# Performance work log

Measured on AMD Instinct MI355X. Metric: run time of the kernel, lower is better.

## Reference

```python
import jax, jax.numpy as jnp
import numpy as np

EMBED_DIM = 400          # d; entity embedding is 2d (alpha|beta)
N_ENTITY = 100000
N_RELATION = 500
HIDDEN = 1600
BATCH = 8192


def _reg(x):
    # Regularizer(base_add=1, min_val=0.05, max_val=1e9)
    return jnp.clip(x + 1.0, 0.05, 1e9)


def setup_inputs() -> dict:
    key = jax.random.key(0)
    ks = jax.random.split(key, 16)
    d = EMBED_DIM
    rng = (9.0 + 2.0) / d  # (gamma + epsilon) / embed_dim with gamma=9

    def xavier(k, shape):
        fan_out, fan_in = shape
        lim = np.sqrt(6.0 / (fan_in + fan_out))
        return jax.random.uniform(k, shape, jnp.float32, -lim, lim)

    inp = {
        "anchor1_idx": jax.random.randint(ks[0], (BATCH,), 0, N_ENTITY),
        "rel1_idx": jax.random.randint(ks[1], (BATCH,), 0, N_RELATION),
        "anchor2_idx": jax.random.randint(ks[2], (BATCH,), 0, N_ENTITY),
        "rel2_idx": jax.random.randint(ks[3], (BATCH,), 0, N_RELATION),
        # embedding tables
        "entity_embedding": jax.random.uniform(ks[4], (N_ENTITY, 2 * d), jnp.float32, -rng, rng),
        "relation_embedding": jax.random.uniform(ks[5], (N_RELATION, d), jnp.float32, -rng, rng),
        # BetaProjection: layer1 [hidden, 2d+d], layer2 [hidden, hidden], layer0 [2d, hidden]
        "pW1": xavier(ks[6], (HIDDEN, 3 * d)),
        "pb1": jnp.zeros((HIDDEN,), jnp.float32),
        "pW2": xavier(ks[7], (HIDDEN, HIDDEN)),
        "pb2": jnp.zeros((HIDDEN,), jnp.float32),
        "pW0": xavier(ks[8], (2 * d, HIDDEN)),
        "pb0": jnp.zeros((2 * d,), jnp.float32),
        # BetaIntersection: layer1 [2d, 2d], layer2 [d, 2d]
        "iW1": xavier(ks[9], (2 * d, 2 * d)),
        "ib1": jnp.zeros((2 * d,), jnp.float32),
        "iW2": xavier(ks[10], (d, 2 * d)),
        "ib2": jnp.zeros((d,), jnp.float32),
    }
    return inp


def _projection(e_emb, r_emb, pW1, pb1, pW2, pb2, pW0, pb0):
    # cat -> Linear+ReLU (layer1) -> Linear+ReLU (layer2) -> layer0 -> regularizer
    x = jnp.concatenate([e_emb, r_emb], axis=-1)           # [B, 3d]
    x = jax.nn.relu(x @ pW1.T + pb1)                       # [B, H]
    x = jax.nn.relu(x @ pW2.T + pb2)                       # [B, H]
    x = x @ pW0.T + pb0                                    # [B, 2d]
    return _reg(x)


def _intersection(alphas, betas, iW1, ib1, iW2, ib2):
    # alphas/betas: [K, B, d]; softmax attention over K
    all_emb = jnp.concatenate([alphas, betas], axis=-1)    # [K, B, 2d]
    h = jax.nn.relu(all_emb @ iW1.T + ib1)                 # [K, B, 2d]
    att = jax.nn.softmax(h @ iW2.T + ib2, axis=0)          # [K, B, d]
    return jnp.sum(att * alphas, axis=0), jnp.sum(att * betas, axis=0)


def reference(anchor1_idx, rel1_idx, anchor2_idx, rel2_idx,
              entity_embedding, relation_embedding,
              pW1, pb1, pW2, pb2, pW0, pb0,
              iW1, ib1, iW2, ib2):
    h = _reg(entity_embedding)                             # entity_regularizer
    r = relation_embedding

    emb1 = _projection(h[anchor1_idx], r[rel1_idx], pW1, pb1, pW2, pb2, pW0, pb0)
    a1, b1 = jnp.split(emb1, 2, axis=-1)
    emb2 = _projection(h[anchor2_idx], r[rel2_idx], pW1, pb1, pW2, pb2, pW0, pb0)
    a2, b2 = jnp.split(emb2, 2, axis=-1)

    alpha, beta = _intersection(jnp.stack([a1, a2]), jnp.stack([b1, b2]),
                                iW1, ib1, iW2, ib2)
    return alpha, beta
```

## Files before the change

### kernel.cpp

```cpp
#include <hip/hip_runtime.h>
#include <hip/hip_bf16.h>
#include <stdint.h>

typedef __bf16 bf16_t;
typedef __bf16 bf16x8 __attribute__((ext_vector_type(8)));
typedef float f32x4 __attribute__((ext_vector_type(4)));

constexpr int BATCH = 8192;
constexpr int M = 2 * BATCH;

constexpr int K1 = 1216;
constexpr int N1c = 1792, N1s = 1664;
constexpr int LDA2 = 1664, KL2 = 1600;
constexpr int N2c = 1792, N2s = 1664;
constexpr int LDA3 = 1664, KL3 = 1600;
constexpr int N3c = 1024, N3s = 1024;
constexpr int LDA4 = 1024, KL4 = 832;
constexpr int N4c = 1024, N4s = 1024;
constexpr int LDA5 = 1024, KL5 = 832, N5 = 512;

__device__ __forceinline__ void gload_lds16(const void* g, void* l) {
  __builtin_amdgcn_global_load_lds(
      (const __attribute__((address_space(1))) void*)g,
      (__attribute__((address_space(3))) void*)l,
      16, 0, 0);
}

#define CFENCE() asm volatile("" ::: "memory")
#define BAR()  { CFENCE(); __builtin_amdgcn_s_barrier(); CFENCE(); }

__global__ void gather_kernel(const int* __restrict__ a1, const int* __restrict__ r1,
                              const int* __restrict__ a2, const int* __restrict__ r2,
                              const float* __restrict__ ent, const float* __restrict__ rel,
                              bf16_t* __restrict__ X) {
  const int row = blockIdx.x;
  const int b   = row & (BATCH - 1);
  const int br  = row >> 13;
  const int eidx = br ? a2[b] : a1[b];
  const int ridx = br ? r2[b] : r1[b];
  const float* __restrict__ esrc = ent + (size_t)eidx * 800;
  const float* __restrict__ rsrc = rel + (size_t)ridx * 400;
  bf16_t* __restrict__ dst = X + (size_t)row * K1;

  for (int g = threadIdx.x; g < K1 / 4; g += 256) {
    const int c = g * 4;
    float4 v = make_float4(0.f, 0.f, 0.f, 0.f);
    if (c < 800) {
      v = *(const float4*)(esrc + c);
      v.x = fminf(fmaxf(v.x + 1.f, 0.05f), 1e9f);
      v.y = fminf(fmaxf(v.y + 1.f, 0.05f), 1e9f);
      v.z = fminf(fmaxf(v.z + 1.f, 0.05f), 1e9f);
      v.w = fminf(fmaxf(v.w + 1.f, 0.05f), 1e9f);
    } else if (c < 1200) {
      v = *(const float4*)(rsrc + (c - 800));
    }
    union { bf16_t h[4]; uint2 u; } pk;
    pk.h[0] = (bf16_t)v.x; pk.h[1] = (bf16_t)v.y;
    pk.h[2] = (bf16_t)v.z; pk.h[3] = (bf16_t)v.w;
    *(uint2*)(dst + c) = pk.u;
  }
}

__device__ __forceinline__ void doconv(int idx, const float* __restrict__ src,
                                       bf16_t* __restrict__ dst, int Nr, int Kc, int Kp) {
  const int kp4 = Kp >> 2;
  const int r = idx / kp4;
  const int c = (idx - r * kp4) << 2;
  union { bf16_t h[4]; uint2 u; } pk;
#pragma unroll
  for (int j = 0; j < 4; ++j) {
    const int cc = c + j;
    const float v = (r < Nr && cc < Kc) ? src[(size_t)r * Kc + cc] : 0.f;
    pk.h[j] = (bf16_t)v;
  }
  *(uint2*)(dst + (size_t)r * Kp + c) = pk.u;
}

constexpr int CJ0 = N1c * K1 / 4;
constexpr int CJ1 = CJ0 + N2c * LDA2 / 4;
constexpr int CJ2 = CJ1 + N3c * LDA3 / 4;
constexpr int CJ3 = CJ2 + N4c * LDA4 / 4;
constexpr int CJ4 = CJ3 + N5 * LDA5 / 4;

__global__ void convw5_kernel(const float* __restrict__ pW1, const float* __restrict__ pW2,
                              const float* __restrict__ pW0, const float* __restrict__ iW1,
                              const float* __restrict__ iW2,
                              bf16_t* __restrict__ W1b, bf16_t* __restrict__ W2b,
                              bf16_t* __restrict__ W0b, bf16_t* __restrict__ iW1b,
                              bf16_t* __restrict__ iW2b) {
  int idx = blockIdx.x * 256 + threadIdx.x;
  if (idx < CJ0)      doconv(idx,        pW1, W1b, 1600, 1200, K1);
  else if (idx < CJ1) doconv(idx - CJ0,  pW2, W2b, 1600, 1600, LDA2);
  else if (idx < CJ2) doconv(idx - CJ1,  pW0, W0b,  800, 1600, LDA3);
  else if (idx < CJ3) doconv(idx - CJ2,  iW1, iW1b, 800,  800, LDA4);
  else                doconv(idx - CJ3,  iW2, iW2b, 400,  800, LDA5);
}

enum { ACT_RELU = 0, ACT_REG = 1, ACT_NONE = 2 };

template <int ACT, int OUTMODE>
__global__ __launch_bounds__(512)
void gemm256(const bf16_t* __restrict__ A, const bf16_t* __restrict__ Bw,
             const float* __restrict__ bias, int Nbias,
             bf16_t* __restrict__ Cb, float* __restrict__ Cf,
             int lda, int Nstore, int NT, int gridN) {
  __shared__ __align__(16) bf16_t lds[8][8192];

  const int nwg = gridDim.x;
  const int id = blockIdx.x;
  const int swz = (id & 7) * (nwg >> 3) + (id >> 3);
  const int bn = swz % gridN, bm = swz / gridN;

  const int t = threadIdx.x;
  const int lane = t & 63;
  const int wv = t >> 6;
  const int wm = wv >> 2, wn = wv & 3;
  const int l15 = lane & 15;
  const int kbs = (((lane >> 4) ^ ((l15 >> 1) & 3)) << 4);

  const int srow = t >> 2;
  const int skc  = (t & 3) ^ ((t >> 3) & 3);
  const bf16_t* aR0 = A  + (size_t)(bm * 256 + srow) * lda + skc * 8;
  const bf16_t* aR1 = aR0 + (size_t)128 * lda;
  const bf16_t* bR0 = Bw + (size_t)(bn * 256 + srow) * lda + skc * 8;
  const bf16_t* bR1 = bR0 + (size_t)128 * lda;
  const int ldsb0 = (wv * 64) * 16;
  const int ldsb1 = (512 + wv * 64) * 16;

  auto STAGE = [&](const bf16_t* r0p, const bf16_t* r1p, int kOff, bf16_t* slot) {
    gload_lds16(r0p + kOff, (char*)slot + ldsb0);
    gload_lds16(r1p + kOff, (char*)slot + ldsb1);
  };

  f32x4 acc[8][4];
#pragma unroll
  for (int i = 0; i < 8; ++i)
#pragma unroll
    for (int j = 0; j < 4; ++j) acc[i][j] = f32x4{0.f, 0.f, 0.f, 0.f};

  STAGE(aR0, aR1, 0, lds[0]);
  STAGE(bR0, bR1, 0, lds[2]);
  STAGE(aR0, aR1, 32, lds[1]);
  STAGE(bR0, bR1, 32, lds[3]);
  if (NT > 1) {
    STAGE(aR0, aR1, 64, lds[4]);
    STAGE(bR0, bR1, 64, lds[6]);
    asm volatile("s_waitcnt vmcnt(8)" ::: "memory");
  } else {
    asm volatile("s_waitcnt vmcnt(4)" ::: "memory");
  }
  __builtin_amdgcn_s_barrier();
  CFENCE();

  bf16x8 bfr[4];
  int db = 0;
  for (int kt = 0; kt < NT; ++kt, db ^= 1) {
    const bool p1 = (kt + 1) < NT;
    const bool p2 = (kt + 2) < NT;
    bf16_t* const cur = (bf16_t*)lds[db * 4];
    bf16_t* const nxt = (bf16_t*)lds[(db ^ 1) * 4];

    {
      const char* sA = (const char*)(cur);
      const char* sB = (const char*)(cur + 2 * 8192);
      bf16x8 af[4];
#pragma unroll
      for (int i = 0; i < 4; ++i)
        af[i] = *(const bf16x8*)(sA + ((wm * 128 + i * 16 + l15) << 6) + kbs);
#pragma unroll
      for (int i = 0; i < 4; ++i)
        bfr[i] = *(const bf16x8*)(sB + ((wn * 64 + i * 16 + l15) << 6) + kbs);
      if (p1) STAGE(aR0, aR1, (kt + 1) * 64 + 32, nxt + 1 * 8192);
      BAR();
      __builtin_amdgcn_s_setprio(1);
#pragma unroll
      for (int i = 0; i < 4; ++i)
#pragma unroll
        for (int j = 0; j < 4; ++j)
          acc[i][j] = __builtin_amdgcn_mfma_f32_16x16x32_bf16(af[i], bfr[j], acc[i][j], 0, 0, 0);
      __builtin_amdgcn_s_setprio(0);
      BAR();
    }
    {
      const char* sA = (const char*)(cur);
      bf16x8 af[4];
#pragma unroll
      for (int i = 0; i < 4; ++i)
        af[i] = *(const bf16x8*)(sA + ((wm * 128 + (4 + i) * 16 + l15) << 6) + kbs);
      if (p1) STAGE(bR0, bR1, (kt + 1) * 64 + 32, nxt + 3 * 8192);
      BAR();
      __builtin_amdgcn_s_setprio(1);
#pragma unroll
      for (int i = 0; i < 4; ++i)
#pragma unroll
        for (int j = 0; j < 4; ++j)
          acc[4 + i][j] = __builtin_amdgcn_mfma_f32_16x16x32_bf16(af[i], bfr[j], acc[4 + i][j], 0, 0, 0);
      __builtin_amdgcn_s_setprio(0);
      if (p1) asm volatile("s_waitcnt vmcnt(8)" ::: "memory");
      else    asm volatile("s_waitcnt vmcnt(0)" ::: "memory");
      BAR();
    }
    {
      const char* sA = (const char*)(cur + 1 * 8192);
      const char* sB = (const char*)(cur + 3 * 8192);
      bf16x8 af[4];
#pragma unroll
      for (int i = 0; i < 4; ++i)
        af[i] = *(const bf16x8*)(sA + ((wm * 128 + i * 16 + l15) << 6) + kbs);
#pragma unroll
      for (int i = 0; i < 4; ++i)
        bfr[i] = *(const bf16x8*)(sB + ((wn * 64 + i * 16 + l15) << 6) + kbs);
      if (p2) STAGE(aR0, aR1, (kt + 2) * 64, cur + 0 * 8192);
      BAR();
      __builtin_amdgcn_s_setprio(1);
#pragma unroll
      for (int i = 0; i < 4; ++i)
#pragma unroll
        for (int j = 0; j < 4; ++j)
          acc[i][j] = __builtin_amdgcn_mfma_f32_16x16x32_bf16(af[i], bfr[j], acc[i][j], 0, 0, 0);
      __builtin_amdgcn_s_setprio(0);
      BAR();
    }
    {
      const char* sA = (const char*)(cur + 1 * 8192);
      bf16x8 af[4];
#pragma unroll
      for (int i = 0; i < 4; ++i)
        af[i] = *(const bf16x8*)(sA + ((wm * 128 + (4 + i) * 16 + l15) << 6) + kbs);
      if (p2) STAGE(bR0, bR1, (kt + 2) * 64, cur + 2 * 8192);
      BAR();
      __builtin_amdgcn_s_setprio(1);
#pragma unroll
      for (int i = 0; i < 4; ++i)
#pragma unroll
        for (int j = 0; j < 4; ++j)
          acc[4 + i][j] = __builtin_amdgcn_mfma_f32_16x16x32_bf16(af[i], bfr[j], acc[4 + i][j], 0, 0, 0);
      __builtin_amdgcn_s_setprio(0);
      if (p1) {
        if (p2) asm volatile("s_waitcnt vmcnt(8)" ::: "memory");
        else    asm volatile("s_waitcnt vmcnt(4)" ::: "memory");
      }
      BAR();
    }
  }

  const int r0 = bm * 256 + wm * 128 + ((lane >> 4) * 4);
  const int c0 = bn * 256 + wn * 64 + l15;
#pragma unroll
  for (int ni = 0; ni < 4; ++ni) {
    const int col = c0 + ni * 16;
    const float bv = (col < Nbias) ? bias[col] : 0.f;
    const bool cok = (col < Nstore);
#pragma unroll
    for (int mi = 0; mi < 8; ++mi) {
#pragma unroll
      for (int j = 0; j < 4; ++j) {
        float v = acc[mi][ni][j] + bv;
        if (ACT == ACT_RELU) v = fmaxf(v, 0.f);
        else if (ACT == ACT_REG) v = fminf(fmaxf(v + 1.f, 0.05f), 1e9f);
        if (cok) {
          const size_t off = (size_t)(r0 + mi * 16 + j) * Nstore + col;
          if (OUTMODE == 0 || OUTMODE == 2) Cb[off] = (bf16_t)v;
          if (OUTMODE == 1 || OUTMODE == 2) Cf[off] = v;
        }
      }
    }
  }
}

template <int ACT, int OUTMODE>
__global__ __launch_bounds__(256)
void gemm_kernel(const bf16_t* __restrict__ A, const bf16_t* __restrict__ Bw,
                 const float* __restrict__ bias, int Nbias,
                 bf16_t* __restrict__ Cb, float* __restrict__ Cf,
                 int lda, int Kloop, int Nd) {
  __shared__ __align__(16) bf16_t As[128 * 64];
  __shared__ __align__(16) bf16_t Bs[128 * 64];

  const int bn = blockIdx.x, bm = blockIdx.y;
  const int t = threadIdx.x;
  const int lane = t & 63;
  const int wv = t >> 6;
  const int wm = wv >> 1, wn = wv & 1;

  f32x4 acc[4][4];
#pragma unroll
  for (int i = 0; i < 4; ++i)
#pragma unroll
    for (int j = 0; j < 4; ++j) acc[i][j] = f32x4{0.f, 0.f, 0.f, 0.f};

  const size_t aBase = (size_t)(bm * 128) * lda;
  const size_t bBase = (size_t)(bn * 128) * lda;

  for (int kt = 0; kt < Kloop; kt += 64) {
    __syncthreads();
#pragma unroll
    for (int q = 0; q < 4; ++q) {
      const int lin = q * 256 + t;
      const int row = lin >> 3;
      const int kc = ((lin & 7) ^ ((lin >> 3) & 7)) * 8;
      const int lofs = (q * 256 + wv * 64) * 16;
      gload_lds16(A + aBase + (size_t)row * lda + kt + kc, (char*)As + lofs);
      gload_lds16(Bw + bBase + (size_t)row * lda + kt + kc, (char*)Bs + lofs);
    }
    __syncthreads();

#pragma unroll
    for (int s = 0; s < 2; ++s) {
      const int crd = s * 4 + (lane >> 4);
      const int k0 = (crd ^ (lane & 7)) * 8;
      bf16x8 af[4], bf[4];
#pragma unroll
      for (int i = 0; i < 4; ++i) {
        const int ra = wm * 64 + i * 16 + (lane & 15);
        af[i] = *(const bf16x8*)(As + ra * 64 + k0);
        const int rb = wn * 64 + i * 16 + (lane & 15);
        bf[i] = *(const bf16x8*)(Bs + rb * 64 + k0);
      }
#pragma unroll
      for (int mi = 0; mi < 4; ++mi)
#pragma unroll
        for (int ni = 0; ni < 4; ++ni)
          acc[mi][ni] = __builtin_amdgcn_mfma_f32_16x16x32_bf16(af[mi], bf[ni], acc[mi][ni], 0, 0, 0);
    }
  }

  const int r0 = bm * 128 + wm * 64 + ((lane >> 4) * 4);
  const int c0 = bn * 128 + wn * 64 + (lane & 15);
#pragma unroll
  for (int ni = 0; ni < 4; ++ni) {
    const int col = c0 + ni * 16;
    const float bv = (col < Nbias) ? bias[col] : 0.f;
#pragma unroll
    for (int mi = 0; mi < 4; ++mi) {
#pragma unroll
      for (int j = 0; j < 4; ++j) {
        float v = acc[mi][ni][j] + bv;
        if (ACT == ACT_RELU) v = fmaxf(v, 0.f);
        else if (ACT == ACT_REG) v = fminf(fmaxf(v + 1.f, 0.05f), 1e9f);
        const size_t off = (size_t)(r0 + mi * 16 + j) * Nd + col;
        if (OUTMODE == 0 || OUTMODE == 2) Cb[off] = (bf16_t)v;
        if (OUTMODE == 1 || OUTMODE == 2) Cf[off] = v;
      }
    }
  }
}

__global__ void combine_kernel(const float* __restrict__ L, const float* __restrict__ E,
                               float* __restrict__ out) {
  const int i = blockIdx.x * 256 + threadIdx.x;
  const int b = i / 400;
  const int d = i - b * 400;
  const float l1 = L[(size_t)b * N5 + d];
  const float l2 = L[(size_t)(BATCH + b) * N5 + d];
  const float att1 = 1.f / (1.f + expf(l2 - l1));
  const float att2 = 1.f - att1;
  const float* E1 = E + (size_t)b * N3s;
  const float* E2 = E + (size_t)(BATCH + b) * N3s;
  out[i] = att1 * E1[d] + att2 * E2[d];
  out[(size_t)BATCH * 400 + i] = att1 * E1[400 + d] + att2 * E2[400 + d];
}

extern "C" void kernel_launch(void* const* d_in, const int* in_sizes, int n_in,
                              void* d_out, int out_size, void* d_ws, size_t ws_size,
                              hipStream_t stream) {
  const int* a1 = (const int*)d_in[0];
  const int* r1 = (const int*)d_in[1];
  const int* a2 = (const int*)d_in[2];
  const int* r2 = (const int*)d_in[3];
  const float* ent = (const float*)d_in[4];
  const float* rel = (const float*)d_in[5];
  const float* pW1 = (const float*)d_in[6];
  const float* pb1 = (const float*)d_in[7];
  const float* pW2 = (const float*)d_in[8];
  const float* pb2 = (const float*)d_in[9];
  const float* pW0 = (const float*)d_in[10];
  const float* pb0 = (const float*)d_in[11];
  const float* iW1 = (const float*)d_in[12];
  const float* ib1 = (const float*)d_in[13];
  const float* iW2 = (const float*)d_in[14];
  const float* ib2 = (const float*)d_in[15];

  char* ws = (char*)d_ws;
  size_t o = 0;
  auto take = [&](size_t bytes) { char* p = ws + o; o += (bytes + 255) & ~(size_t)255; return p; };
  bf16_t* W1b  = (bf16_t*)take((size_t)N1c * K1 * 2);
  bf16_t* W2b  = (bf16_t*)take((size_t)N2c * LDA2 * 2);
  bf16_t* W0b  = (bf16_t*)take((size_t)N3c * LDA3 * 2);
  bf16_t* iW1b = (bf16_t*)take((size_t)N4c * LDA4 * 2);
  bf16_t* iW2b = (bf16_t*)take((size_t)N5 * LDA5 * 2);
  char* bufX = take((size_t)M * K1 * 2);
  char* bufY = take((size_t)M * N1s * 2);
  char* bufZ = take((size_t)M * N2s * 2);
  float* Ef  = (float*)take((size_t)M * N3s * 4);

  bf16_t* Xb = (bf16_t*)bufX;
  bf16_t* Yb = (bf16_t*)bufY;
  bf16_t* Zb = (bf16_t*)bufZ;
  bf16_t* Eb = (bf16_t*)bufX;
  bf16_t* Hb = (bf16_t*)bufY;
  float*  Lf = (float*)bufZ;

  convw5_kernel<<<dim3(CJ4 / 256), 256, 0, stream>>>(pW1, pW2, pW0, iW1, iW2,
                                                     W1b, W2b, W0b, iW1b, iW2b);

  gather_kernel<<<M, 256, 0, stream>>>(a1, r1, a2, r2, ent, rel, Xb);

  gemm256<ACT_RELU, 0><<<dim3((N1c / 256) * (M / 256)), 512, 0, stream>>>(
      Xb, W1b, pb1, 1600, Yb, nullptr, K1, N1s, K1 / 64, N1c / 256);
  gemm256<ACT_RELU, 0><<<dim3((N2c / 256) * (M / 256)), 512, 0, stream>>>(
      Yb, W2b, pb2, 1600, Zb, nullptr, LDA2, N2s, KL2 / 64, N2c / 256);
  gemm256<ACT_REG, 2><<<dim3((N3c / 256) * (M / 256)), 512, 0, stream>>>(
      Zb, W0b, pb0, 800, Eb, Ef, LDA3, N3s, KL3 / 64, N3c / 256);
  gemm256<ACT_RELU, 0><<<dim3((N4c / 256) * (M / 256)), 512, 0, stream>>>(
      Eb, iW1b, ib1, 800, Hb, nullptr, LDA4, N4s, KL4 / 64, N4c / 256);
  gemm_kernel<ACT_NONE, 1><<<dim3(N5 / 128, M / 128), 256, 0, stream>>>(
      Hb, iW2b, ib2, 400, nullptr, Lf, LDA5, KL5, N5);

  combine_kernel<<<(BATCH * 400) / 256, 256, 0, stream>>>(Lf, Ef, (float*)d_out);
}
```

Measured before the change: 367.8 us.

## Fuse final GEMM with softmax combine, merge prep kernels, drop fp32 E buffer

Merges the gather and weight-conversion kernels into one launch. The last intersection GEMM now computes both branches' logits in the same block and applies the two-way softmax and weighted sum directly in its epilogue, so the fp32 logits buffer and the separate combine kernel go away. The REG GEMM now writes only bf16 E instead of both bf16 and fp32, and stores are limited to the valid columns rather than the padded ones. This removes launches and intermediate global traffic, but the combine reads E in bf16, which lowers precision, and the fused epilogue reads E with scattered accesses.

```diff
diff --git a/kernel.cpp b/kernel.cpp
--- a/kernel.cpp
+++ b/kernel.cpp
@@ -10,13 +10,17 @@
 constexpr int M = 2 * BATCH;
 
 constexpr int K1 = 1216;
-constexpr int N1c = 1792, N1s = 1664;
+constexpr int N1c = 1792;
+constexpr int LDC1 = 1664, NS1 = 1600;
 constexpr int LDA2 = 1664, KL2 = 1600;
-constexpr int N2c = 1792, N2s = 1664;
+constexpr int N2c = 1792;
+constexpr int LDC2 = 1664, NS2 = 1600;
 constexpr int LDA3 = 1664, KL3 = 1600;
-constexpr int N3c = 1024, N3s = 1024;
+constexpr int N3c = 1024;
+constexpr int LDC3 = 1024, NS3 = 832;
 constexpr int LDA4 = 1024, KL4 = 832;
-constexpr int N4c = 1024, N4s = 1024;
+constexpr int N4c = 1024;
+constexpr int LDC4 = 1024, NS4 = 832;
 constexpr int LDA5 = 1024, KL5 = 832, N5 = 512;
 
 __device__ __forceinline__ void gload_lds16(const void* g, void* l) {
@@ -28,38 +32,6 @@
 
 #define CFENCE() asm volatile("" ::: "memory")
 #define BAR()  { CFENCE(); __builtin_amdgcn_s_barrier(); CFENCE(); }
-
-__global__ void gather_kernel(const int* __restrict__ a1, const int* __restrict__ r1,
-                              const int* __restrict__ a2, const int* __restrict__ r2,
-                              const float* __restrict__ ent, const float* __restrict__ rel,
-                              bf16_t* __restrict__ X) {
-  const int row = blockIdx.x;
-  const int b   = row & (BATCH - 1);
-  const int br  = row >> 13;
-  const int eidx = br ? a2[b] : a1[b];
-  const int ridx = br ? r2[b] : r1[b];
-  const float* __restrict__ esrc = ent + (size_t)eidx * 800;
-  const float* __restrict__ rsrc = rel + (size_t)ridx * 400;
-  bf16_t* __restrict__ dst = X + (size_t)row * K1;
-
-  for (int g = threadIdx.x; g < K1 / 4; g += 256) {
-    const int c = g * 4;
-    float4 v = make_float4(0.f, 0.f, 0.f, 0.f);
-    if (c < 800) {
-      v = *(const float4*)(esrc + c);
-      v.x = fminf(fmaxf(v.x + 1.f, 0.05f), 1e9f);
-      v.y = fminf(fmaxf(v.y + 1.f, 0.05f), 1e9f);
-      v.z = fminf(fmaxf(v.z + 1.f, 0.05f), 1e9f);
-      v.w = fminf(fmaxf(v.w + 1.f, 0.05f), 1e9f);
-    } else if (c < 1200) {
-      v = *(const float4*)(rsrc + (c - 800));
-    }
-    union { bf16_t h[4]; uint2 u; } pk;
-    pk.h[0] = (bf16_t)v.x; pk.h[1] = (bf16_t)v.y;
-    pk.h[2] = (bf16_t)v.z; pk.h[3] = (bf16_t)v.w;
-    *(uint2*)(dst + c) = pk.u;
-  }
-}
 
 __device__ __forceinline__ void doconv(int idx, const float* __restrict__ src,
                                        bf16_t* __restrict__ dst, int Nr, int Kc, int Kp) {
@@ -81,29 +53,63 @@
 constexpr int CJ2 = CJ1 + N3c * LDA3 / 4;
 constexpr int CJ3 = CJ2 + N4c * LDA4 / 4;
 constexpr int CJ4 = CJ3 + N5 * LDA5 / 4;
-
-__global__ void convw5_kernel(const float* __restrict__ pW1, const float* __restrict__ pW2,
-                              const float* __restrict__ pW0, const float* __restrict__ iW1,
-                              const float* __restrict__ iW2,
-                              bf16_t* __restrict__ W1b, bf16_t* __restrict__ W2b,
-                              bf16_t* __restrict__ W0b, bf16_t* __restrict__ iW1b,
-                              bf16_t* __restrict__ iW2b) {
-  int idx = blockIdx.x * 256 + threadIdx.x;
-  if (idx < CJ0)      doconv(idx,        pW1, W1b, 1600, 1200, K1);
-  else if (idx < CJ1) doconv(idx - CJ0,  pW2, W2b, 1600, 1600, LDA2);
-  else if (idx < CJ2) doconv(idx - CJ1,  pW0, W0b,  800, 1600, LDA3);
-  else if (idx < CJ3) doconv(idx - CJ2,  iW1, iW1b, 800,  800, LDA4);
-  else                doconv(idx - CJ3,  iW2, iW2b, 400,  800, LDA5);
-}
-
-enum { ACT_RELU = 0, ACT_REG = 1, ACT_NONE = 2 };
-
-template <int ACT, int OUTMODE>
+constexpr int CONV_BLOCKS = CJ4 / 256;
+constexpr int PREP_BLOCKS = M + CONV_BLOCKS;
+
+__global__ void prep_kernel(const int* __restrict__ a1, const int* __restrict__ r1,
+                            const int* __restrict__ a2, const int* __restrict__ r2,
+                            const float* __restrict__ ent, const float* __restrict__ rel,
+                            bf16_t* __restrict__ X,
+                            const float* __restrict__ pW1, const float* __restrict__ pW2,
+                            const float* __restrict__ pW0, const float* __restrict__ iW1,
+                            const float* __restrict__ iW2,
+                            bf16_t* __restrict__ W1b, bf16_t* __restrict__ W2b,
+                            bf16_t* __restrict__ W0b, bf16_t* __restrict__ iW1b,
+                            bf16_t* __restrict__ iW2b) {
+  if (blockIdx.x < M) {
+    const int row = blockIdx.x;
+    const int b   = row & (BATCH - 1);
+    const int br  = row >> 13;
+    const int eidx = br ? a2[b] : a1[b];
+    const int ridx = br ? r2[b] : r1[b];
+    const float* __restrict__ esrc = ent + (size_t)eidx * 800;
+    const float* __restrict__ rsrc = rel + (size_t)ridx * 400;
+    bf16_t* __restrict__ dst = X + (size_t)row * K1;
+    for (int g = threadIdx.x; g < K1 / 4; g += 256) {
+      const int c = g * 4;
+      float4 v = make_float4(0.f, 0.f, 0.f, 0.f);
+      if (c < 800) {
+        v = *(const float4*)(esrc + c);
+        v.x = fminf(fmaxf(v.x + 1.f, 0.05f), 1e9f);
+        v.y = fminf(fmaxf(v.y + 1.f, 0.05f), 1e9f);
+        v.z = fminf(fmaxf(v.z + 1.f, 0.05f), 1e9f);
+        v.w = fminf(fmaxf(v.w + 1.f, 0.05f), 1e9f);
+      } else if (c < 1200) {
+        v = *(const float4*)(rsrc + (c - 800));
+      }
+      union { bf16_t h[4]; uint2 u; } pk;
+      pk.h[0] = (bf16_t)v.x; pk.h[1] = (bf16_t)v.y;
+      pk.h[2] = (bf16_t)v.z; pk.h[3] = (bf16_t)v.w;
+      *(uint2*)(dst + c) = pk.u;
+    }
+  } else {
+    const int idx = (blockIdx.x - M) * 256 + threadIdx.x;
+    if (idx < CJ0)      doconv(idx,        pW1, W1b, 1600, 1200, K1);
+    else if (idx < CJ1) doconv(idx - CJ0,  pW2, W2b, 1600, 1600, LDA2);
+    else if (idx < CJ2) doconv(idx - CJ1,  pW0, W0b,  800, 1600, LDA3);
+    else if (idx < CJ3) doconv(idx - CJ2,  iW1, iW1b, 800,  800, LDA4);
+    else if (idx < CJ4) doconv(idx - CJ3,  iW2, iW2b, 400,  800, LDA5);
+  }
+}
+
+enum { ACT_RELU = 0, ACT_REG = 1 };
+
+template <int ACT>
 __global__ __launch_bounds__(512)
 void gemm256(const bf16_t* __restrict__ A, const bf16_t* __restrict__ Bw,
              const float* __restrict__ bias, int Nbias,
-             bf16_t* __restrict__ Cb, float* __restrict__ Cf,
-             int lda, int Nstore, int NT, int gridN) {
+             bf16_t* __restrict__ Cb,
+             int lda, int Nstore, int ldc, int NT, int gridN) {
   __shared__ __align__(16) bf16_t lds[8][8192];
 
   const int nwg = gridDim.x;
@@ -257,24 +263,19 @@
       for (int j = 0; j < 4; ++j) {
         float v = acc[mi][ni][j] + bv;
         if (ACT == ACT_RELU) v = fmaxf(v, 0.f);
-        else if (ACT == ACT_REG) v = fminf(fmaxf(v + 1.f, 0.05f), 1e9f);
-        if (cok) {
-          const size_t off = (size_t)(r0 + mi * 16 + j) * Nstore + col;
-          if (OUTMODE == 0 || OUTMODE == 2) Cb[off] = (bf16_t)v;
-          if (OUTMODE == 1 || OUTMODE == 2) Cf[off] = v;
-        }
+        else                 v = fminf(fmaxf(v + 1.f, 0.05f), 1e9f);
+        if (cok) Cb[(size_t)(r0 + mi * 16 + j) * ldc + col] = (bf16_t)v;
       }
     }
   }
 }
 
-template <int ACT, int OUTMODE>
 __global__ __launch_bounds__(256)
-void gemm_kernel(const bf16_t* __restrict__ A, const bf16_t* __restrict__ Bw,
-                 const float* __restrict__ bias, int Nbias,
-                 bf16_t* __restrict__ Cb, float* __restrict__ Cf,
-                 int lda, int Kloop, int Nd) {
-  __shared__ __align__(16) bf16_t As[128 * 64];
+void g5_combine(const bf16_t* __restrict__ H, const bf16_t* __restrict__ Wb,
+                const float* __restrict__ ib2, const bf16_t* __restrict__ E,
+                float* __restrict__ out) {
+  __shared__ __align__(16) bf16_t As1[128 * 64];
+  __shared__ __align__(16) bf16_t As2[128 * 64];
   __shared__ __align__(16) bf16_t Bs[128 * 64];
 
   const int bn = blockIdx.x, bm = blockIdx.y;
@@ -283,25 +284,27 @@
   const int wv = t >> 6;
   const int wm = wv >> 1, wn = wv & 1;
 
-  f32x4 acc[4][4];
+  f32x4 acc1[4][4], acc2[4][4];
 #pragma unroll
   for (int i = 0; i < 4; ++i)
 #pragma unroll
-    for (int j = 0; j < 4; ++j) acc[i][j] = f32x4{0.f, 0.f, 0.f, 0.f};
-
-  const size_t aBase = (size_t)(bm * 128) * lda;
-  const size_t bBase = (size_t)(bn * 128) * lda;
-
-  for (int kt = 0; kt < Kloop; kt += 64) {
+    for (int j = 0; j < 4; ++j) { acc1[i][j] = f32x4{0.f,0.f,0.f,0.f}; acc2[i][j] = f32x4{0.f,0.f,0.f,0.f}; }
+
+  const size_t a1Base = (size_t)(bm * 128) * LDA5;
+  const size_t a2Base = (size_t)(8192 + bm * 128) * LDA5;
+  const size_t bBase  = (size_t)(bn * 128) * LDA5;
+
+  for (int kt = 0; kt < KL5; kt += 64) {
     __syncthreads();
 #pragma unroll
     for (int q = 0; q < 4; ++q) {
       const int lin = q * 256 + t;
       const int row = lin >> 3;
-      const int kc = ((lin & 7) ^ ((lin >> 3) & 7)) * 8;
+      const int kc = ((lin & 7) ^ (row & 7)) * 8;
       const int lofs = (q * 256 + wv * 64) * 16;
-      gload_lds16(A + aBase + (size_t)row * lda + kt + kc, (char*)As + lofs);
-      gload_lds16(Bw + bBase + (size_t)row * lda + kt + kc, (char*)Bs + lofs);
+      gload_lds16(H + a1Base + (size_t)row * LDA5 + kt + kc, (char*)As1 + lofs);
+      gload_lds16(H + a2Base + (size_t)row * LDA5 + kt + kc, (char*)As2 + lofs);
+      gload_lds16(Wb + bBase + (size_t)row * LDA5 + kt + kc, (char*)Bs + lofs);
     }
     __syncthreads();
 
@@ -309,56 +312,50 @@
     for (int s = 0; s < 2; ++s) {
       const int crd = s * 4 + (lane >> 4);
       const int k0 = (crd ^ (lane & 7)) * 8;
-      bf16x8 af[4], bf[4];
+      bf16x8 af1[4], af2[4], bf[4];
 #pragma unroll
       for (int i = 0; i < 4; ++i) {
         const int ra = wm * 64 + i * 16 + (lane & 15);
-        af[i] = *(const bf16x8*)(As + ra * 64 + k0);
+        af1[i] = *(const bf16x8*)(As1 + ra * 64 + k0);
+        af2[i] = *(const bf16x8*)(As2 + ra * 64 + k0);
         const int rb = wn * 64 + i * 16 + (lane & 15);
         bf[i] = *(const bf16x8*)(Bs + rb * 64 + k0);
       }
 #pragma unroll
       for (int mi = 0; mi < 4; ++mi)
 #pragma unroll
-        for (int ni = 0; ni < 4; ++ni)
-          acc[mi][ni] = __builtin_amdgcn_mfma_f32_16x16x32_bf16(af[mi], bf[ni], acc[mi][ni], 0, 0, 0);
-    }
-  }
-
-  const int r0 = bm * 128 + wm * 64 + ((lane >> 4) * 4);
-  const int c0 = bn * 128 + wn * 64 + (lane & 15);
+        for (int ni = 0; ni < 4; ++ni) {
+          acc1[mi][ni] = __builtin_amdgcn_mfma_f32_16x16x32_bf16(af1[mi], bf[ni], acc1[mi][ni], 0, 0, 0);
+          acc2[mi][ni] = __builtin_amdgcn_mfma_f32_16x16x32_bf16(af2[mi], bf[ni], acc2[mi][ni], 0, 0, 0);
+        }
+    }
+  }
+
+  const int rloc0 = wm * 64 + ((lane >> 4) * 4);
+  const int cloc0 = wn * 64 + (lane & 15);
 #pragma unroll
   for (int ni = 0; ni < 4; ++ni) {
-    const int col = c0 + ni * 16;
-    const float bv = (col < Nbias) ? bias[col] : 0.f;
+    const int d = bn * 128 + cloc0 + ni * 16;
+    if (d >= 400) continue;
+    const float bv = ib2[d];
 #pragma unroll
     for (int mi = 0; mi < 4; ++mi) {
 #pragma unroll
       for (int j = 0; j < 4; ++j) {
-        float v = acc[mi][ni][j] + bv;
-        if (ACT == ACT_RELU) v = fmaxf(v, 0.f);
-        else if (ACT == ACT_REG) v = fminf(fmaxf(v + 1.f, 0.05f), 1e9f);
-        const size_t off = (size_t)(r0 + mi * 16 + j) * Nd + col;
-        if (OUTMODE == 0 || OUTMODE == 2) Cb[off] = (bf16_t)v;
-        if (OUTMODE == 1 || OUTMODE == 2) Cf[off] = v;
+        const int b = bm * 128 + rloc0 + mi * 16 + j;
+        const float l1 = acc1[mi][ni][j] + bv;
+        const float l2 = acc2[mi][ni][j] + bv;
+        const float att1 = 1.f / (1.f + expf(l2 - l1));
+        const float att2 = 1.f - att1;
+        const bf16_t* E1 = E + (size_t)b * LDC3;
+        const bf16_t* E2 = E + (size_t)(8192 + b) * LDC3;
+        out[(size_t)b * 400 + d] =
+            att1 * (float)E1[d] + att2 * (float)E2[d];
+        out[(size_t)8192 * 400 + (size_t)b * 400 + d] =
+            att1 * (float)E1[400 + d] + att2 * (float)E2[400 + d];
       }
     }
   }
-}
-
-__global__ void combine_kernel(const float* __restrict__ L, const float* __restrict__ E,
-                               float* __restrict__ out) {
-  const int i = blockIdx.x * 256 + threadIdx.x;
-  const int b = i / 400;
-  const int d = i - b * 400;
-  const float l1 = L[(size_t)b * N5 + d];
-  const float l2 = L[(size_t)(BATCH + b) * N5 + d];
-  const float att1 = 1.f / (1.f + expf(l2 - l1));
-  const float att2 = 1.f - att1;
-  const float* E1 = E + (size_t)b * N3s;
-  const float* E2 = E + (size_t)(BATCH + b) * N3s;
-  out[i] = att1 * E1[d] + att2 * E2[d];
-  out[(size_t)BATCH * 400 + i] = att1 * E1[400 + d] + att2 * E2[400 + d];
 }
 
 extern "C" void kernel_launch(void* const* d_in, const int* in_sizes, int n_in,
@@ -390,32 +387,27 @@
   bf16_t* iW1b = (bf16_t*)take((size_t)N4c * LDA4 * 2);
   bf16_t* iW2b = (bf16_t*)take((size_t)N5 * LDA5 * 2);
   char* bufX = take((size_t)M * K1 * 2);
-  char* bufY = take((size_t)M * N1s * 2);
-  char* bufZ = take((size_t)M * N2s * 2);
-  float* Ef  = (float*)take((size_t)M * N3s * 4);
+  char* bufY = take((size_t)M * LDC1 * 2);
+  char* bufZ = take((size_t)M * LDC2 * 2);
 
   bf16_t* Xb = (bf16_t*)bufX;
   bf16_t* Yb = (bf16_t*)bufY;
   bf16_t* Zb = (bf16_t*)bufZ;
   bf16_t* Eb = (bf16_t*)bufX;
   bf16_t* Hb = (bf16_t*)bufY;
-  float*  Lf = (float*)bufZ;
-
-  convw5_kernel<<<dim3(CJ4 / 256), 256, 0, stream>>>(pW1, pW2, pW0, iW1, iW2,
+
+  prep_kernel<<<dim3(PREP_BLOCKS), 256, 0, stream>>>(a1, r1, a2, r2, ent, rel, Xb,
+                                                     pW1, pW2, pW0, iW1, iW2,
                                                      W1b, W2b, W0b, iW1b, iW2b);
 
-  gather_kernel<<<M, 256, 0, stream>>>(a1, r1, a2, r2, ent, rel, Xb);
-
-  gemm256<ACT_RELU, 0><<<dim3((N1c / 256) * (M / 256)), 512, 0, stream>>>(
-      Xb, W1b, pb1, 1600, Yb, nullptr, K1, N1s, K1 / 64, N1c / 256);
-  gemm256<ACT_RELU, 0><<<dim3((N2c / 256) * (M / 256)), 512, 0, stream>>>(
-      Yb, W2b, pb2, 1600, Zb, nullptr, LDA2, N2s, KL2 / 64, N2c / 256);
-  gemm256<ACT_REG, 2><<<dim3((N3c / 256) * (M / 256)), 512, 0, stream>>>(
-      Zb, W0b, pb0, 800, Eb, Ef, LDA3, N3s, KL3 / 64, N3c / 256);
-  gemm256<ACT_RELU, 0><<<dim3((N4c / 256) * (M / 256)), 512, 0, stream>>>(
-      Eb, iW1b, ib1, 800, Hb, nullptr, LDA4, N4s, KL4 / 64, N4c / 256);
-  gemm_kernel<ACT_NONE, 1><<<dim3(N5 / 128, M / 128), 256, 0, stream>>>(
-      Hb, iW2b, ib2, 400, nullptr, Lf, LDA5, KL5, N5);
-
-  combine_kernel<<<(BATCH * 400) / 256, 256, 0, stream>>>(Lf, Ef, (float*)d_out);
-}
+  gemm256<ACT_RELU><<<dim3((N1c / 256) * (M / 256)), 512, 0, stream>>>(
+      Xb, W1b, pb1, 1600, Yb, K1, NS1, LDC1, K1 / 64, N1c / 256);
+  gemm256<ACT_RELU><<<dim3((N2c / 256) * (M / 256)), 512, 0, stream>>>(
+      Yb, W2b, pb2, 1600, Zb, LDA2, NS2, LDC2, KL2 / 64, N2c / 256);
+  gemm256<ACT_REG><<<dim3((N3c / 256) * (M / 256)), 512, 0, stream>>>(
+      Zb, W0b, pb0, 800, Eb, LDA3, NS3, LDC3, KL3 / 64, N3c / 256);
+  gemm256<ACT_RELU><<<dim3((N4c / 256) * (M / 256)), 512, 0, stream>>>(
+      Eb, iW1b, ib1, 800, Hb, LDA4, NS4, LDC4, KL4 / 64, N4c / 256);
+  g5_combine<<<dim3(N5 / 128, BATCH / 128), 256, 0, stream>>>(
+      Hb, iW2b, ib2, Eb, (float*)d_out);
+}
```

After: 348.7 us. 1.05x faster.
